# Kernel tuning notes

Measured on AMD Instinct MI355X. Metric: run time of the kernel, lower is better.

The kernel has to match this reference:

```python
import jax, jax.numpy as jnp
import numpy as np

HEADS = 4
DIM_HEAD = 32


def setup_inputs() -> dict:
    key = jax.random.key(0)
    k1, k2, k3 = jax.random.split(key, 3)
    B, L, D = 16, 8192, 256
    hidden = HEADS * DIM_HEAD  # 128
    x = jax.random.normal(k1, (B, L, D), dtype=jnp.float32)
    W_qkv = jax.random.normal(k2, (D, 3 * hidden), dtype=jnp.float32) * (D ** -0.5)
    W_out = jax.random.normal(k3, (hidden, D), dtype=jnp.float32) * (hidden ** -0.5)
    b_out = jnp.zeros((D,), dtype=jnp.float32)
    return {"x": x, "W_qkv": W_qkv, "W_out": W_out, "b_out": b_out}


def reference(x, W_qkv, W_out, b_out):
    B, L, D = x.shape
    scale = DIM_HEAD ** -0.5
    # 1x1 conv == per-token matmul
    qkv = jnp.einsum('bld,df->blf', x, W_qkv)  # [B, L, 3*h*dh]
    qkv = qkv.reshape(B, L, 3, HEADS, DIM_HEAD)
    q = jnp.transpose(qkv[:, :, 0], (0, 2, 1, 3)) * scale          # [B, h, L, d]
    k = jax.nn.softmax(jnp.transpose(qkv[:, :, 1], (0, 2, 1, 3)), axis=2)  # softmax over L
    v = jnp.transpose(qkv[:, :, 2], (0, 2, 1, 3))                  # [B, h, L, e]
    context = jnp.einsum('bhld,bhle->bhde', k, v)                  # [B, h, d, e]
    out = jnp.einsum('bhde,bhld->bhle', context, q)                # [B, h, L, e]
    out = jnp.transpose(out, (0, 2, 1, 3)).reshape(B, L, HEADS * DIM_HEAD)
    return jnp.einsum('blf,fd->bld', out, W_out) + b_out
```

## Files before the change

### kernel.cpp

```cpp
#include <hip/hip_runtime.h>
#include <math.h>


typedef __attribute__((ext_vector_type(8))) short bf16x8;
typedef __attribute__((ext_vector_type(4))) float f32x4;
typedef __attribute__((ext_vector_type(4))) unsigned u32x4;

__device__ __forceinline__ unsigned cvt_pk2(float a, float b) {
    unsigned r;
    asm("v_cvt_pk_bf16_f32 %0, %1, %2" : "=v"(r) : "v"(a), "v"(b));
    return r;
}
__device__ __forceinline__ ushort bf16_rn(float f) {
    return (ushort)cvt_pk2(f, f);
}
__device__ __forceinline__ float bf16f(ushort h) { return __uint_as_float(((unsigned)h) << 16); }

__device__ __forceinline__ void glds16(const void* g, void* l) {
    __builtin_amdgcn_global_load_lds((const __attribute__((address_space(1))) unsigned int*)g,
                                     (__attribute__((address_space(3))) unsigned int*)l,
                                     16, 0, 0);
}

__global__ __launch_bounds__(256) void prep_kernel(const float* __restrict__ W,
                                                   ushort* __restrict__ wh,
                                                   ushort* __restrict__ wl) {
    int n = blockIdx.x, k = threadIdx.x;
    float f = W[k * 384 + 128 + n];
    ushort h = bf16_rn(f);
    wh[n * 256 + k] = h;
    wl[n * 256 + k] = bf16_rn(f - bf16f(h));
}

__global__ __launch_bounds__(256) void gemm_kv(
    const float* __restrict__ X,
    const ushort* __restrict__ Wh, const ushort* __restrict__ Wl,
    float* __restrict__ S_part, float* __restrict__ Z_part) {
    __shared__ __align__(16) char smem[66560];
    float*  As  = (float*)smem;
    ushort* Bsh = (ushort*)(smem + 8192);
    ushort* Bsl = (ushort*)(smem + 8192 + 16384);
    float*  tile = (float*)smem;

    const int tid = threadIdx.x;
    const int blk = blockIdx.x;
    const long row0 = (long)blk * 64;
    const int lane = tid & 63, wave = tid >> 6;
    const int wc = wave * 64;
    const int m = lane & 15, quad = lane >> 4;
    const int ra = lane >> 3, pa = lane & 7;
    const int rb = lane >> 2, pb = lane & 3;

    f32x4 acc[4][4] = {};

    for (int k0 = 0; k0 < 256; k0 += 32) {
#pragma unroll
        for (int s = 0; s < 2; ++s) {
            int seg = s * 4 + wave;
            int r = seg * 8 + ra;
            int q = pa ^ (r & 7);
            glds16(&X[(row0 + r) * 256 + k0 + q * 4], &As[seg * 256]);
        }
#pragma unroll
        for (int s = 0; s < 4; ++s) {
            int seg = s * 4 + wave;
            int r = seg * 16 + rb;
            int q = pb ^ ((r >> 1) & 3);
            glds16(&Wh[r * 256 + k0 + q * 8], &Bsh[seg * 512]);
            glds16(&Wl[r * 256 + k0 + q * 8], &Bsl[seg * 512]);
        }
        __syncthreads();

        bf16x8 bh[4], bl[4];
#pragma unroll
        for (int j = 0; j < 4; ++j) {
            int r = wc + j * 16 + m;
            int p = quad ^ ((r >> 1) & 3);
            bh[j] = *(const bf16x8*)&Bsh[r * 32 + p * 8];
            bl[j] = *(const bf16x8*)&Bsl[r * 32 + p * 8];
        }
#pragma unroll
        for (int i = 0; i < 4; ++i) {
            int r = i * 16 + m;
            int p0 = (quad * 2) ^ (r & 7);
            int p1 = (quad * 2 + 1) ^ (r & 7);
            f32x4 a0 = *(const f32x4*)&As[r * 32 + p0 * 4];
            f32x4 a1 = *(const f32x4*)&As[r * 32 + p1 * 4];
            u32x4 ahw, alw;
#pragma unroll
            for (int e = 0; e < 2; ++e) {
                float f0 = a0[2 * e], f1 = a0[2 * e + 1];
                unsigned h = cvt_pk2(f0, f1);
                ahw[e] = h;
                alw[e] = cvt_pk2(f0 - __uint_as_float(h << 16),
                                 f1 - __uint_as_float(h & 0xFFFF0000u));
            }
#pragma unroll
            for (int e = 0; e < 2; ++e) {
                float f0 = a1[2 * e], f1 = a1[2 * e + 1];
                unsigned h = cvt_pk2(f0, f1);
                ahw[2 + e] = h;
                alw[2 + e] = cvt_pk2(f0 - __uint_as_float(h << 16),
                                     f1 - __uint_as_float(h & 0xFFFF0000u));
            }
            bf16x8 ah = __builtin_bit_cast(bf16x8, ahw);
            bf16x8 al = __builtin_bit_cast(bf16x8, alw);
#pragma unroll
            for (int j = 0; j < 4; ++j) {
                acc[i][j] = __builtin_amdgcn_mfma_f32_16x16x32_bf16(ah, bh[j], acc[i][j], 0, 0, 0);
                acc[i][j] = __builtin_amdgcn_mfma_f32_16x16x32_bf16(ah, bl[j], acc[i][j], 0, 0, 0);
                acc[i][j] = __builtin_amdgcn_mfma_f32_16x16x32_bf16(al, bh[j], acc[i][j], 0, 0, 0);
            }
        }
        __syncthreads();
    }

#pragma unroll
    for (int i = 0; i < 4; ++i)
#pragma unroll
        for (int r4 = 0; r4 < 4; ++r4) {
            int rl = i * 16 + quad * 4 + r4;
#pragma unroll
            for (int j = 0; j < 4; ++j) {
                int c = wc + j * 16 + m;
                float v = acc[i][j][r4];
                tile[rl * 260 + c] = (c < 128) ? __expf(v) : v;
            }
        }
    __syncthreads();

    const int h = wave, d = lane >> 1, eg = lane & 1, e0 = eg * 16;
    float sacc[16] = {};
    float z = 0.f;
#pragma unroll 4
    for (int l = 0; l < 64; ++l) {
        const float* rowp = &tile[l * 260];
        float ek = rowp[h * 32 + d];
        const f32x4* vp = (const f32x4*)&rowp[128 + h * 32 + e0];
        f32x4 v0 = vp[0], v1 = vp[1], v2 = vp[2], v3 = vp[3];
        z += ek;
        sacc[0]  += ek * v0[0]; sacc[1]  += ek * v0[1]; sacc[2]  += ek * v0[2]; sacc[3]  += ek * v0[3];
        sacc[4]  += ek * v1[0]; sacc[5]  += ek * v1[1]; sacc[6]  += ek * v1[2]; sacc[7]  += ek * v1[3];
        sacc[8]  += ek * v2[0]; sacc[9]  += ek * v2[1]; sacc[10] += ek * v2[2]; sacc[11] += ek * v2[3];
        sacc[12] += ek * v3[0]; sacc[13] += ek * v3[1]; sacc[14] += ek * v3[2]; sacc[15] += ek * v3[3];
    }
    long sb = (long)blk * 4096 + h * 1024 + d * 32 + e0;
#pragma unroll
    for (int t = 0; t < 16; ++t) S_part[sb + t] = sacc[t];
    if (eg == 0) Z_part[blk * 128 + h * 32 + d] = z;
}

__global__ __launch_bounds__(256) void combine_kernel(const float* __restrict__ S_part,
                                                      const float* __restrict__ Z_part,
                                                      const float* __restrict__ Wout,
                                                      float* __restrict__ m2f) {
    int bh = blockIdx.x;
    int b = bh >> 2, h = bh & 3;
    int n = threadIdx.x;
    __shared__ float ctx[32][33];
    __shared__ float zs[32];
    if (n < 32) {
        float z = 0.f;
        for (int j = 0; j < 128; ++j) z += Z_part[(b * 128 + j) * 128 + h * 32 + n];
        zs[n] = z;
    }
    float s4[4] = {};
    for (int j = 0; j < 128; ++j) {
        const float* sp = &S_part[((long)(b * 128 + j)) * 4096 + h * 1024];
#pragma unroll
        for (int t = 0; t < 4; ++t) s4[t] += sp[t * 256 + n];
    }
    __syncthreads();
#pragma unroll
    for (int t = 0; t < 4; ++t) {
        int idx = t * 256 + n;
        ctx[idx >> 5][idx & 31] = s4[t] / zs[idx >> 5];
    }
    __syncthreads();
    const float scale = 0.17677669529663687f;
    float acc[32];
#pragma unroll
    for (int dd = 0; dd < 32; ++dd) acc[dd] = 0.f;
    for (int e = 0; e < 32; ++e) {
        float w = Wout[(h * 32 + e) * 256 + n];
#pragma unroll
        for (int dd = 0; dd < 32; ++dd) acc[dd] += ctx[dd][e] * w;
    }
#pragma unroll
    for (int dd = 0; dd < 32; ++dd)
        m2f[((long)(b * 128 + h * 32 + dd)) * 256 + n] = acc[dd] * scale;
}

__global__ __launch_bounds__(256) void w2eff_kernel(const float* __restrict__ Wqkv,
                                                    const float* __restrict__ m2f,
                                                    ushort* __restrict__ w2h,
                                                    ushort* __restrict__ w2l) {
    int bid = blockIdx.x;
    int b = bid >> 4, kg = bid & 15;
    int n = threadIdx.x;
    __shared__ float lWq[16 * 128];
#pragma unroll
    for (int u = 0; u < 8; ++u) {
        int idx = u * 256 + n;
        int k = idx >> 7, hd = idx & 127;
        lWq[idx] = Wqkv[(kg * 16 + k) * 384 + hd];
    }
    __syncthreads();
    float acc[16] = {};
    for (int hd = 0; hd < 128; ++hd) {
        float mm = m2f[((long)(b * 128 + hd)) * 256 + n];
#pragma unroll
        for (int k = 0; k < 16; ++k) acc[k] += lWq[k * 128 + hd] * mm;
    }
    long base = ((long)(b * 256 + n)) * 256 + kg * 16;
#pragma unroll
    for (int k = 0; k < 16; ++k) {
        ushort hh = bf16_rn(acc[k]);
        w2h[base + k] = hh;
        w2l[base + k] = bf16_rn(acc[k] - bf16f(hh));
    }
}

__global__ __launch_bounds__(256) void gemm2_kernel(
    const float* __restrict__ X,
    const ushort* __restrict__ W2h, const ushort* __restrict__ W2l,
    const float* __restrict__ bias, float* __restrict__ out) {
    __shared__ __align__(16) float  As[4096];
    __shared__ __align__(16) ushort Bsh[4096];
    __shared__ __align__(16) ushort Bsl[4096];
    const int tid = threadIdx.x;
    const int wg = blockIdx.x;
    const int xcd = wg & 7;
    const int u = wg >> 3;
    const int cbl = u & 1;
    const int gid = (u >> 1) * 8 + xcd;
    const long bz = gid >> 6;
    const int row0 = (gid & 63) * 128;
    const int col0 = cbl * 128;
    const float* Xb = X + bz * (8192L * 256);
    const ushort* Bh = W2h + bz * (256L * 256);
    const ushort* Bl = W2l + bz * (256L * 256);
    const int lane = tid & 63, wave = tid >> 6;
    const int wr = (wave & 1) * 64, wc = (wave >> 1) * 64;
    const int m = lane & 15, quad = lane >> 4;
    const int ra = lane >> 3, pa = lane & 7;
    const int rb = lane >> 2, pb = lane & 3;

    f32x4 acc[4][4] = {};

    for (int k0 = 0; k0 < 256; k0 += 32) {
#pragma unroll
        for (int s = 0; s < 4; ++s) {
            int seg = s * 4 + wave;
            int r = seg * 8 + ra;
            int q = pa ^ (r & 7);
            glds16(&Xb[(long)(row0 + r) * 256 + k0 + q * 4], &As[seg * 256]);
        }
#pragma unroll
        for (int s = 0; s < 2; ++s) {
            int seg = s * 4 + wave;
            int r = seg * 16 + rb;
            int q = pb ^ ((r >> 1) & 3);
            glds16(&Bh[(col0 + r) * 256 + k0 + q * 8], &Bsh[seg * 512]);
            glds16(&Bl[(col0 + r) * 256 + k0 + q * 8], &Bsl[seg * 512]);
        }
        __syncthreads();

        bf16x8 bh[4], bl[4];
#pragma unroll
        for (int j = 0; j < 4; ++j) {
            int r = wc + j * 16 + m;
            int p = quad ^ ((r >> 1) & 3);
            bh[j] = *(const bf16x8*)&Bsh[r * 32 + p * 8];
            bl[j] = *(const bf16x8*)&Bsl[r * 32 + p * 8];
        }
#pragma unroll
        for (int i = 0; i < 4; ++i) {
            int r = wr + i * 16 + m;
            int p0 = (quad * 2) ^ (r & 7);
            int p1 = (quad * 2 + 1) ^ (r & 7);
            f32x4 a0 = *(const f32x4*)&As[r * 32 + p0 * 4];
            f32x4 a1 = *(const f32x4*)&As[r * 32 + p1 * 4];
            u32x4 ahw, alw;
#pragma unroll
            for (int e = 0; e < 2; ++e) {
                float f0 = a0[2 * e], f1 = a0[2 * e + 1];
                unsigned h = cvt_pk2(f0, f1);
                ahw[e] = h;
                alw[e] = cvt_pk2(f0 - __uint_as_float(h << 16),
                                 f1 - __uint_as_float(h & 0xFFFF0000u));
            }
#pragma unroll
            for (int e = 0; e < 2; ++e) {
                float f0 = a1[2 * e], f1 = a1[2 * e + 1];
                unsigned h = cvt_pk2(f0, f1);
                ahw[2 + e] = h;
                alw[2 + e] = cvt_pk2(f0 - __uint_as_float(h << 16),
                                     f1 - __uint_as_float(h & 0xFFFF0000u));
            }
            bf16x8 ah = __builtin_bit_cast(bf16x8, ahw);
            bf16x8 al = __builtin_bit_cast(bf16x8, alw);
#pragma unroll
            for (int j = 0; j < 4; ++j) {
                acc[i][j] = __builtin_amdgcn_mfma_f32_16x16x32_bf16(ah, bh[j], acc[i][j], 0, 0, 0);
                acc[i][j] = __builtin_amdgcn_mfma_f32_16x16x32_bf16(ah, bl[j], acc[i][j], 0, 0, 0);
                acc[i][j] = __builtin_amdgcn_mfma_f32_16x16x32_bf16(al, bh[j], acc[i][j], 0, 0, 0);
            }
        }
        __syncthreads();
    }

    float bv[4];
#pragma unroll
    for (int j = 0; j < 4; ++j) bv[j] = bias[col0 + wc + j * 16 + m];
    float* outb = out + bz * (8192L * 256);
#pragma unroll
    for (int i = 0; i < 4; ++i)
#pragma unroll
        for (int r4 = 0; r4 < 4; ++r4) {
            long row = row0 + wr + i * 16 + quad * 4 + r4;
#pragma unroll
            for (int j = 0; j < 4; ++j)
                outb[row * 256 + col0 + wc + j * 16 + m] = acc[i][j][r4] + bv[j];
        }
}

extern "C" void kernel_launch(void* const* d_in, const int* in_sizes, int n_in,
                              void* d_out, int out_size, void* d_ws, size_t ws_size,
                              hipStream_t stream) {
    const float* x     = (const float*)d_in[0];
    const float* W_qkv = (const float*)d_in[1];
    const float* W_out = (const float*)d_in[2];
    const float* b_out = (const float*)d_in[3];
    float* out = (float*)d_out;

    char* p = (char*)d_ws;
    ushort* wth = (ushort*)p; p += 256 * 256 * 2;
    ushort* wtl = (ushort*)p; p += 256 * 256 * 2;
    float* Sp   = (float*)p;  p += (long)2048 * 4096 * 4;
    float* Zp   = (float*)p;  p += 2048 * 128 * 4;
    float* m2f  = (float*)p;  p += 16 * 128 * 256 * 4;
    ushort* w2h = (ushort*)p; p += (long)16 * 256 * 256 * 2;
    ushort* w2l = (ushort*)p; p += (long)16 * 256 * 256 * 2;

    prep_kernel<<<256, 256, 0, stream>>>(W_qkv, wth, wtl);
    gemm_kv<<<2048, 256, 0, stream>>>(x, wth, wtl, Sp, Zp);
    combine_kernel<<<64, 256, 0, stream>>>(Sp, Zp, W_out, m2f);
    w2eff_kernel<<<256, 256, 0, stream>>>(W_qkv, m2f, w2h, w2l);
    gemm2_kernel<<<2048, 256, 0, stream>>>(x, w2h, w2l, b_out, out);
}
```

Measured before the change: 382.1 us.

## Halve gemm_kv epilogue LDS tile and parallelize partial-sum reduction

The gemm_kv epilogue now writes the exp(K)/V tile in two 32-row halves, which cuts shared memory from 66560 to 40960 bytes so more blocks can reside per CU. The cross-block reduction of the S/Z partials moves out of the 64-block combine kernel into a new 256-block reduce_parts kernel, so the partial sums are read by many more threads in parallel. This adds one kernel launch, one extra barrier in gemm_kv, and a small workspace round trip.

```diff
diff --git a/kernel.cpp b/kernel.cpp
--- a/kernel.cpp
+++ b/kernel.cpp
@@ -36,7 +36,7 @@
     const float* __restrict__ X,
     const ushort* __restrict__ Wh, const ushort* __restrict__ Wl,
     float* __restrict__ S_part, float* __restrict__ Z_part) {
-    __shared__ __align__(16) char smem[66560];
+    __shared__ __align__(16) char smem[40960];
     float*  As  = (float*)smem;
     ushort* Bsh = (ushort*)(smem + 8192);
     ushort* Bsl = (ushort*)(smem + 8192 + 16384);
@@ -115,34 +115,38 @@
         __syncthreads();
     }
 
-#pragma unroll
-    for (int i = 0; i < 4; ++i)
-#pragma unroll
-        for (int r4 = 0; r4 < 4; ++r4) {
-            int rl = i * 16 + quad * 4 + r4;
-#pragma unroll
-            for (int j = 0; j < 4; ++j) {
-                int c = wc + j * 16 + m;
-                float v = acc[i][j][r4];
-                tile[rl * 260 + c] = (c < 128) ? __expf(v) : v;
-            }
-        }
-    __syncthreads();
-
     const int h = wave, d = lane >> 1, eg = lane & 1, e0 = eg * 16;
     float sacc[16] = {};
     float z = 0.f;
+    for (int half = 0; half < 2; ++half) {
+        if (half) __syncthreads();
+#pragma unroll
+        for (int ii = 0; ii < 2; ++ii) {
+            int i = half * 2 + ii;
+#pragma unroll
+            for (int r4 = 0; r4 < 4; ++r4) {
+                int rl = ii * 16 + quad * 4 + r4;
+#pragma unroll
+                for (int j = 0; j < 4; ++j) {
+                    int c = wc + j * 16 + m;
+                    float v = acc[i][j][r4];
+                    tile[rl * 260 + c] = (c < 128) ? __expf(v) : v;
+                }
+            }
+        }
+        __syncthreads();
 #pragma unroll 4
-    for (int l = 0; l < 64; ++l) {
-        const float* rowp = &tile[l * 260];
-        float ek = rowp[h * 32 + d];
-        const f32x4* vp = (const f32x4*)&rowp[128 + h * 32 + e0];
-        f32x4 v0 = vp[0], v1 = vp[1], v2 = vp[2], v3 = vp[3];
-        z += ek;
-        sacc[0]  += ek * v0[0]; sacc[1]  += ek * v0[1]; sacc[2]  += ek * v0[2]; sacc[3]  += ek * v0[3];
-        sacc[4]  += ek * v1[0]; sacc[5]  += ek * v1[1]; sacc[6]  += ek * v1[2]; sacc[7]  += ek * v1[3];
-        sacc[8]  += ek * v2[0]; sacc[9]  += ek * v2[1]; sacc[10] += ek * v2[2]; sacc[11] += ek * v2[3];
-        sacc[12] += ek * v3[0]; sacc[13] += ek * v3[1]; sacc[14] += ek * v3[2]; sacc[15] += ek * v3[3];
+        for (int l = 0; l < 32; ++l) {
+            const float* rowp = &tile[l * 260];
+            float ek = rowp[h * 32 + d];
+            const f32x4* vp = (const f32x4*)&rowp[128 + h * 32 + e0];
+            f32x4 v0 = vp[0], v1 = vp[1], v2 = vp[2], v3 = vp[3];
+            z += ek;
+            sacc[0]  += ek * v0[0]; sacc[1]  += ek * v0[1]; sacc[2]  += ek * v0[2]; sacc[3]  += ek * v0[3];
+            sacc[4]  += ek * v1[0]; sacc[5]  += ek * v1[1]; sacc[6]  += ek * v1[2]; sacc[7]  += ek * v1[3];
+            sacc[8]  += ek * v2[0]; sacc[9]  += ek * v2[1]; sacc[10] += ek * v2[2]; sacc[11] += ek * v2[3];
+            sacc[12] += ek * v3[0]; sacc[13] += ek * v3[1]; sacc[14] += ek * v3[2]; sacc[15] += ek * v3[3];
+        }
     }
     long sb = (long)blk * 4096 + h * 1024 + d * 32 + e0;
 #pragma unroll
@@ -150,8 +154,29 @@
     if (eg == 0) Z_part[blk * 128 + h * 32 + d] = z;
 }
 
-__global__ __launch_bounds__(256) void combine_kernel(const float* __restrict__ S_part,
-                                                      const float* __restrict__ Z_part,
+__global__ __launch_bounds__(256) void reduce_parts(const float* __restrict__ Sp,
+                                                    const float* __restrict__ Zp,
+                                                    float* __restrict__ S,
+                                                    float* __restrict__ Z) {
+    int g = blockIdx.x * 256 + threadIdx.x;
+    int b = g >> 12, idx = g & 4095;
+    const float* p = Sp + ((long)b * 128) * 4096 + idx;
+    float s0 = 0.f, s1 = 0.f;
+#pragma unroll 4
+    for (int j = 0; j < 64; ++j) { s0 += p[j * 4096]; s1 += p[(j + 64) * 4096]; }
+    S[g] = s0 + s1;
+    if (g < 2048) {
+        int bb = g >> 7, c = g & 127;
+        const float* q = Zp + (long)bb * 128 * 128 + c;
+        float z0 = 0.f, z1 = 0.f;
+#pragma unroll 4
+        for (int j = 0; j < 64; ++j) { z0 += q[j * 128]; z1 += q[(j + 64) * 128]; }
+        Z[g] = z0 + z1;
+    }
+}
+
+__global__ __launch_bounds__(256) void combine_kernel(const float* __restrict__ S,
+                                                      const float* __restrict__ Z,
                                                       const float* __restrict__ Wout,
                                                       float* __restrict__ m2f) {
     int bh = blockIdx.x;
@@ -159,22 +184,12 @@
     int n = threadIdx.x;
     __shared__ float ctx[32][33];
     __shared__ float zs[32];
-    if (n < 32) {
-        float z = 0.f;
-        for (int j = 0; j < 128; ++j) z += Z_part[(b * 128 + j) * 128 + h * 32 + n];
-        zs[n] = z;
-    }
-    float s4[4] = {};
-    for (int j = 0; j < 128; ++j) {
-        const float* sp = &S_part[((long)(b * 128 + j)) * 4096 + h * 1024];
-#pragma unroll
-        for (int t = 0; t < 4; ++t) s4[t] += sp[t * 256 + n];
-    }
+    if (n < 32) zs[n] = Z[b * 128 + h * 32 + n];
     __syncthreads();
 #pragma unroll
     for (int t = 0; t < 4; ++t) {
         int idx = t * 256 + n;
-        ctx[idx >> 5][idx & 31] = s4[t] / zs[idx >> 5];
+        ctx[idx >> 5][idx & 31] = S[(long)b * 4096 + h * 1024 + idx] / zs[idx >> 5];
     }
     __syncthreads();
     const float scale = 0.17677669529663687f;
@@ -339,13 +354,16 @@
     ushort* wtl = (ushort*)p; p += 256 * 256 * 2;
     float* Sp   = (float*)p;  p += (long)2048 * 4096 * 4;
     float* Zp   = (float*)p;  p += 2048 * 128 * 4;
+    float* Sr   = (float*)p;  p += 16 * 4096 * 4;
+    float* Zr   = (float*)p;  p += 2048 * 4;
     float* m2f  = (float*)p;  p += 16 * 128 * 256 * 4;
     ushort* w2h = (ushort*)p; p += (long)16 * 256 * 256 * 2;
     ushort* w2l = (ushort*)p; p += (long)16 * 256 * 256 * 2;
 
     prep_kernel<<<256, 256, 0, stream>>>(W_qkv, wth, wtl);
     gemm_kv<<<2048, 256, 0, stream>>>(x, wth, wtl, Sp, Zp);
-    combine_kernel<<<64, 256, 0, stream>>>(Sp, Zp, W_out, m2f);
+    reduce_parts<<<256, 256, 0, stream>>>(Sp, Zp, Sr, Zr);
+    combine_kernel<<<64, 256, 0, stream>>>(Sr, Zr, W_out, m2f);
     w2eff_kernel<<<256, 256, 0, stream>>>(W_qkv, m2f, w2h, w2l);
     gemm2_kernel<<<2048, 256, 0, stream>>>(x, w2h, w2l, b_out, out);
 }
```

After: 388.5 us. About the same (+1.7%).
